# Kernel tuning notes

Hardware: AMD Instinct MI355X
Metric: run time of the kernel (lower is better)

## Reference

```python
import jax, jax.numpy as jnp
import numpy as np

N_VARS = 100_000
N_CLAUSES = 420_000
NNZ = 3 * N_CLAUSES
N_GRAPHS = 32
FM = 64
QM = 64
ROUNDS = 8
EPS = 1e-6


def _dense_init(key, din, dout):
    lim = float(np.sqrt(6.0 / (din + dout)))
    W = jax.random.uniform(key, (din, dout), jnp.float32, -lim, lim)
    return W, jnp.zeros((dout,), jnp.float32)


def setup_inputs() -> dict:
    key = jax.random.key(0)
    ks = jax.random.split(key, 16)
    # sparse literal-clause incidence: 3 literals per clause (3-SAT)
    lit_idx = jax.random.randint(ks[0], (NNZ,), 0, 2 * N_VARS)
    clause_idx = jnp.repeat(jnp.arange(N_CLAUSES), 3)
    # graph membership (batched formulas), contiguous per graph
    var_gid = jnp.sort(jax.random.randint(ks[1], (N_VARS,), 0, N_GRAPHS))
    clause_gid = jnp.sort(jax.random.randint(ks[2], (N_CLAUSES,), 0, N_GRAPHS))
    inp = {"lit_idx": lit_idx, "clause_idx": clause_idx,
           "var_gid": var_gid, "clause_gid": clause_gid}
    dims = {
        "vq": [(FM + 4, QM), (QM, QM)],                       # variables_query
        "cm": [(2 * FM, 2 * FM), (2 * FM, FM + QM)],          # clause_update
        "ug": [(4 * FM, 2 * FM), (2 * FM, 2 * FM), (2 * FM, FM)],  # update_gate
        "co": [(FM, FM), (FM, 1)],                             # clauses_mask_output
    }
    i = 3
    for name, layers in dims.items():
        for l, (din, dout) in enumerate(layers):
            W, b = _dense_init(ks[i], din, dout)
            i += 1
            inp[f"{name}_W{l}"] = W
            inp[f"{name}_b{l}"] = b
    return inp


def _mlp(x, params):
    for W, b in params[:-1]:
        x = jax.nn.relu(x @ W + b)
    W, b = params[-1]
    return x @ W + b


def _pair_norm(x, gid, n_graphs):
    # per-graph mean-subtract + RMS normalize (PairNorm, subtract_mean=True)
    cnt = jnp.maximum(
        jax.ops.segment_sum(jnp.ones((x.shape[0],), x.dtype), gid, num_segments=n_graphs), 1.0)[:, None]
    mean = jax.ops.segment_sum(x, gid, num_segments=n_graphs) / cnt
    x = x - mean[gid]
    var = jax.ops.segment_sum(jnp.mean(x * x, axis=-1, keepdims=True), gid, num_segments=n_graphs) / cnt
    return x * jax.lax.rsqrt(var[gid] + EPS)


def _forward(lit_idx, clause_idx, var_gid, clause_gid,
             vq_W0, vq_b0, vq_W1, vq_b1,
             cm_W0, cm_b0, cm_W1, cm_b1,
             ug_W0, ug_b0, ug_W1, ug_b1, ug_W2, ug_b2,
             co_W0, co_b0, co_W1, co_b1):
    vq = [(vq_W0, vq_b0), (vq_W1, vq_b1)]
    cm = [(cm_W0, cm_b0), (cm_W1, cm_b1)]
    ug = [(ug_W0, ug_b0), (ug_W1, ug_b1), (ug_W2, ug_b2)]
    co = [(co_W0, co_b0), (co_W1, co_b1)]
    V = var_gid.shape[0]
    C = clause_gid.shape[0]
    L = 2 * V  # literals

    variables = jnp.ones((V, FM), jnp.float32)
    clauses = jnp.ones((C, FM), jnp.float32)

    ones_e = jnp.ones((lit_idx.shape[0],), jnp.float32)
    lit_degree = jax.ops.segment_sum(ones_e, lit_idx, num_segments=L)[:, None]  # [2V,1]
    degree_weight = jax.lax.rsqrt(jnp.maximum(lit_degree, 1.0))
    var_degree_weight = 4.0 * jax.lax.rsqrt(jnp.maximum(lit_degree[:V] + lit_degree[V:], 1.0))

    def clause_loss(q):
        # softplus_loss_adj: exp(-(adj^T @ softplus([q; -q])))
        lits = jax.nn.softplus(jnp.concatenate([q, -q], axis=0))  # [2V, QM]
        cv = jax.ops.segment_sum(lits[lit_idx], clause_idx, num_segments=C)  # [C, QM]
        cl = jnp.exp(-cv)
        return jnp.sum(cl), cl

    def body(carry, key):
        variables, clauses = carry
        v1 = jnp.concatenate(
            [variables, jax.random.normal(key, (V, 4), jnp.float32)], axis=-1)
        query = _mlp(v1, vq)  # [V, QM]
        (_, clauses_loss), q_grad = jax.value_and_grad(clause_loss, has_aux=True)(query)
        variables_grad = q_grad * var_degree_weight

        clause_unit = jnp.concatenate([clauses, 4.0 * clauses_loss], axis=-1)  # [C, 2*FM]
        clause_data = _mlp(clause_unit, cm)  # [C, FM+QM]
        variables_loss_all = clause_data[:, :QM]
        new_clause = _pair_norm(clause_data[:, QM:], clause_gid, N_GRAPHS) * 0.25
        clauses = new_clause + 0.1 * clauses

        # adj @ variables_loss_all : scatter clause features to literals
        variables_loss = jax.ops.segment_sum(
            variables_loss_all[clause_idx], lit_idx, num_segments=L) * degree_weight  # [2V, QM]
        unit = jnp.concatenate(
            [variables_grad, variables, variables_loss[:V], variables_loss[V:]], axis=-1)
        new_variables = _pair_norm(_mlp(unit, ug), var_gid, N_GRAPHS) * 0.25
        variables = new_variables + 0.1 * variables

        logits = _mlp(clauses, co)  # [C, 1]
        variables = jax.lax.stop_gradient(variables) * 0.2 + variables * 0.8
        clauses = jax.lax.stop_gradient(clauses) * 0.2  # + clauses * 0.0
        return (variables, clauses), logits

    keys = jax.random.split(jax.random.key(42), ROUNDS + 1)
    (_, _), logits_seq = jax.lax.scan(body, (variables, clauses), keys[:ROUNDS])
    last_logits = logits_seq[-1]
    noise = jax.random.normal(keys[ROUNDS], last_logits.shape, jnp.float32)
    return jnp.squeeze(jax.nn.sigmoid(last_logits + noise), axis=-1)  # [C]


def reference(lit_idx, clause_idx, var_gid, clause_gid,
              vq_W0, vq_b0, vq_W1, vq_b1,
              cm_W0, cm_b0, cm_W1, cm_b1,
              ug_W0, ug_b0, ug_W1, ug_b1, ug_W2, ug_b2,
              co_W0, co_b0, co_W1, co_b1):
    return _forward(lit_idx, clause_idx, var_gid, clause_gid,
                    vq_W0, vq_b0, vq_W1, vq_b1,
                    cm_W0, cm_b0, cm_W1, cm_b1,
                    ug_W0, ug_b0, ug_W1, ug_b1, ug_W2, ug_b2,
                    co_W0, co_b0, co_W1, co_b1)
```

## Files before the change

### kernel.cpp

```cpp
#include <hip/hip_runtime.h>
#include <hip/hip_bf16.h>
#include <cstdint>
#include <cstddef>

constexpr int V_N = 100000;
constexpr int C_N = 420000;
constexpr int L_N = 2 * V_N;
constexpr int E_N = 3 * C_N;
constexpr int NGR = 32;
constexpr int NROUNDS = 8;
constexpr int SCAN_NB = (L_N + 255) / 256;

using bf16 = __hip_bfloat16;
typedef __attribute__((ext_vector_type(8))) short short8;
typedef __attribute__((ext_vector_type(4))) float float4v;

__device__ inline float b2f(bf16 h) { return __bfloat162float(h); }
__device__ inline bf16 f2b(float f) { return __float2bfloat16(f); }
__device__ inline float sb2f(short s) { return __uint_as_float(((uint32_t)(uint16_t)s) << 16); }
__device__ inline short f2sb(float f) { bf16 h = f2b(f); return *(short*)&h; }

template<typename T> __device__ inline float loadT(const T* p);
template<> __device__ inline float loadT<float>(const float* p) { return *p; }
template<> __device__ inline float loadT<bf16>(const bf16* p) { return b2f(*p); }

template<typename TX> __device__ inline void load8(const TX* p, float* v);
template<> __device__ inline void load8<bf16>(const bf16* p, float* v) {
  short8 s = *(const short8*)p;
#pragma unroll
  for (int e = 0; e < 8; e++) v[e] = sb2f(s[e]);
}
template<> __device__ inline void load8<float>(const float* p, float* v) {
  float4 a = *(const float4*)p;
  float4 b = *(const float4*)(p + 4);
  v[0] = a.x; v[1] = a.y; v[2] = a.z; v[3] = a.w;
  v[4] = b.x; v[5] = b.y; v[6] = b.z; v[7] = b.w;
}

__device__ inline float wload(const void* W, size_t idx, int isf32) {
  return isf32 ? ((const float*)W)[idx] : b2f(((const bf16*)W)[idx]);
}

__host__ __device__ inline void tf2x32(uint32_t k0, uint32_t k1,
                                       uint32_t x0, uint32_t x1,
                                       uint32_t* o0, uint32_t* o1) {
  uint32_t ks2 = k0 ^ k1 ^ 0x1BD11BDAu;
  x0 += k0; x1 += k1;
#define TFR(d) do { x0 += x1; x1 = (x1 << (d)) | (x1 >> (32 - (d))); x1 ^= x0; } while (0)
  TFR(13); TFR(15); TFR(26); TFR(6);
  x0 += k1;  x1 += ks2 + 1u;
  TFR(17); TFR(29); TFR(16); TFR(24);
  x0 += ks2; x1 += k0 + 2u;
  TFR(13); TFR(15); TFR(26); TFR(6);
  x0 += k0;  x1 += k1 + 3u;
  TFR(17); TFR(29); TFR(16); TFR(24);
  x0 += k1;  x1 += ks2 + 4u;
  TFR(13); TFR(15); TFR(26); TFR(6);
  x0 += ks2; x1 += k0 + 5u;
#undef TFR
  *o0 = x0; *o1 = x1;
}

__device__ inline uint32_t part_bits(uint32_t ka, uint32_t kb, uint32_t e) {
  uint32_t h1, h2;
  tf2x32(ka, kb, 0u, e, &h1, &h2);
  return h1 ^ h2;
}

__device__ inline float erfinv_f32(float x) {
  float w = -log1pf(-x * x);
  float p;
  if (w < 5.0f) {
    w -= 2.5f;
    p = 2.81022636e-08f;
    p = fmaf(p, w, 3.43273939e-07f);
    p = fmaf(p, w, -3.5233877e-06f);
    p = fmaf(p, w, -4.39150654e-06f);
    p = fmaf(p, w, 0.00021858087f);
    p = fmaf(p, w, -0.00125372503f);
    p = fmaf(p, w, -0.00417768164f);
    p = fmaf(p, w, 0.246640727f);
    p = fmaf(p, w, 1.50140941f);
  } else {
    w = sqrtf(w) - 3.0f;
    p = -0.000200214257f;
    p = fmaf(p, w, 0.000100950558f);
    p = fmaf(p, w, 0.00134934322f);
    p = fmaf(p, w, -0.00367342844f);
    p = fmaf(p, w, 0.00573950773f);
    p = fmaf(p, w, -0.0076224613f);
    p = fmaf(p, w, 0.00943887047f);
    p = fmaf(p, w, 1.00167406f);
    p = fmaf(p, w, 2.83297682f);
  }
  return p * x;
}

__device__ inline float normal_from_bits(uint32_t bits) {
  float u01 = __uint_as_float((bits >> 9) | 0x3f800000u) - 1.0f;
  const float lo = -0.99999994f;
  float u = u01 * 2.0f + lo;
  u = fmaxf(lo, u);
  return 1.41421356f * erfinv_f32(u);
}

__global__ void fill_f32(float* p, size_t n, float v) {
  size_t i = (size_t)blockIdx.x * blockDim.x + threadIdx.x;
  size_t stride = (size_t)gridDim.x * blockDim.x;
  for (; i < n; i += stride) p[i] = v;
}
__global__ void fill_u32(uint32_t* p, size_t n, uint32_t v) {
  size_t i = (size_t)blockIdx.x * blockDim.x + threadIdx.x;
  size_t stride = (size_t)gridDim.x * blockDim.x;
  for (; i < n; i += stride) p[i] = v;
}
__global__ void fill_b16(bf16* p, size_t n, float v) {
  size_t i = (size_t)blockIdx.x * blockDim.x + threadIdx.x;
  size_t stride = (size_t)gridDim.x * blockDim.x;
  bf16 b = f2b(v);
  for (; i < n; i += stride) p[i] = b;
}

__global__ void detect_dtype_kernel(const uint32_t* __restrict__ w, int* __restrict__ flag) {
  if (blockIdx.x == 0 && threadIdx.x == 0) {
    int votes = 0;
    for (int i = 0; i < 16; i++) {
      uint32_t lo = w[i] & 0xFFFFu;
      uint32_t e = (lo >> 7) & 0xFFu;
      if (e >= 0x70u && e < 0x80u) votes++;
    }
    *flag = (votes >= 12) ? 0 : 1;
  }
}

__global__ void pack_w_kernel(const void* __restrict__ W, const int* __restrict__ flagp,
                              int realK, int Kpad, int M, int Wld, int wcol0,
                              int srow0, float sscale, bf16* __restrict__ out) {
  int idx = blockIdx.x * 256 + threadIdx.x;
  if (idx >= Kpad * M) return;
  int j = idx & 7;
  int lane = (idx >> 3) & 63;
  int t = idx >> 9;
  int MT = M / 16;
  int kt = t / MT, nt = t - kt * MT;
  int k = kt * 32 + (lane >> 4) * 8 + j;
  int n = nt * 16 + (lane & 15);
  float v = 0.0f;
  if (k < realK) {
    v = wload(W, (size_t)k * Wld + wcol0 + n, *flagp);
    if (k >= srow0) v *= sscale;
  }
  out[idx] = f2b(v);
}

__global__ void count_deg_kernel(const int* __restrict__ lit, int* __restrict__ deg) {
  int e = blockIdx.x * 256 + threadIdx.x;
  if (e < E_N) atomicAdd(&deg[lit[e]], 1);
}

__global__ void hist32_kernel(const int* __restrict__ gid, int n, int* __restrict__ out) {
  __shared__ int bins[NGR];
  int t = threadIdx.x;
  if (t < NGR) bins[t] = 0;
  __syncthreads();
  int i = blockIdx.x * 256 + t;
  if (i < n) atomicAdd(&bins[gid[i]], 1);
  __syncthreads();
  if (t < NGR && bins[t] > 0) atomicAdd(&out[t], bins[t]);
}

__global__ void weights_kernel(const int* __restrict__ deg,
                               float* __restrict__ dw, float* __restrict__ vdw) {
  int l = blockIdx.x * 256 + threadIdx.x;
  if (l < L_N) dw[l] = rsqrtf(fmaxf((float)deg[l], 1.0f));
  if (l < V_N) vdw[l] = 4.0f * rsqrtf(fmaxf((float)(deg[l] + deg[l + V_N]), 1.0f));
}

__global__ void scan_partial_kernel(const int* __restrict__ deg, int* __restrict__ part) {
  __shared__ int red[256];
  int b = blockIdx.x, t = threadIdx.x;
  int i = b * 256 + t;
  red[t] = (i < L_N) ? deg[i] : 0;
  __syncthreads();
  for (int o = 128; o > 0; o >>= 1) {
    if (t < o) red[t] += red[t + o];
    __syncthreads();
  }
  if (t == 0) part[b] = red[0];
}

__global__ void scan_base_kernel(const int* __restrict__ part, int* __restrict__ base) {
  __shared__ int buf[SCAN_NB + 1];
  int t = threadIdx.x;
  for (int i = t; i < SCAN_NB; i += 256) buf[i] = part[i];
  __syncthreads();
  if (t == 0) {
    int acc = 0;
    for (int i = 0; i < SCAN_NB; i++) { int v = buf[i]; buf[i] = acc; acc += v; }
    buf[SCAN_NB] = acc;
  }
  __syncthreads();
  for (int i = t; i <= SCAN_NB; i += 256) base[i] = buf[i];
}

__global__ void scan_write_kernel(const int* __restrict__ deg, const int* __restrict__ base,
                                  int* __restrict__ offs) {
  __shared__ int s[256];
  int b = blockIdx.x, t = threadIdx.x;
  int i = b * 256 + t;
  int v = (i < L_N) ? deg[i] : 0;
  s[t] = v;
  __syncthreads();
  for (int o = 1; o < 256; o <<= 1) {
    int x = (t >= o) ? s[t - o] : 0;
    __syncthreads();
    s[t] += x;
    __syncthreads();
  }
  if (i < L_N) offs[i] = base[b] + s[t] - v;
  if (b == 0 && t == 0) offs[L_N] = base[SCAN_NB];
}

__global__ void csr_fill_kernel(const int* __restrict__ lit,
                                const int* __restrict__ offs, int* __restrict__ cursor,
                                int* __restrict__ csr) {
  int e = blockIdx.x * 256 + threadIdx.x;
  if (e < E_N) {
    int l = lit[e];
    int p = atomicAdd(&cursor[l], 1);
    csr[offs[l] + p] = e / 3;
  }
}


__global__ __launch_bounds__(256) void vq_fused_kernel(
    const bf16* __restrict__ variables,
    const bf16* __restrict__ W0p, const void* __restrict__ b0,
    const bf16* __restrict__ W1p, const void* __restrict__ b1,
    const int* __restrict__ flagp, uint32_t ka, uint32_t kb,
    bf16* __restrict__ SG, int N) {
  __shared__ bf16 hs[64][72];
  int tid = threadIdx.x;
  int wave = tid >> 6, lane = tid & 63, quad = lane >> 4, m16 = lane & 15;
  int row = blockIdx.x * 64 + wave * 16 + m16;
  int rowc = min(row, N - 1);
  int isf32 = *flagp;
  float4v acc[4];
#pragma unroll
  for (int nt = 0; nt < 4; nt++) acc[nt] = (float4v){0.f, 0.f, 0.f, 0.f};
  const short8* w0 = (const short8*)W0p;
  for (int k0 = 0; k0 < 96; k0 += 32) {
    int ks = k0 + quad * 8;
    short8 a;
    if (ks < 64) {
      a = *(const short8*)(variables + (size_t)rowc * 64 + ks);
    } else if (ks == 64) {
#pragma unroll
      for (int e = 0; e < 8; e++)
        a[e] = (e < 4)
             ? f2sb(normal_from_bits(part_bits(ka, kb, (uint32_t)(rowc * 4 + e))))
             : (short)0;
    } else {
      a = (short8){0, 0, 0, 0, 0, 0, 0, 0};
    }
#pragma unroll
    for (int nt = 0; nt < 4; nt++) {
      short8 b = w0[((k0 >> 5) * 4 + nt) * 64 + lane];
      acc[nt] = __builtin_amdgcn_mfma_f32_16x16x32_bf16(a, b, acc[nt], 0, 0, 0);
    }
  }
  int rl = wave * 16 + quad * 4;
#pragma unroll
  for (int nt = 0; nt < 4; nt++) {
    int col = nt * 16 + m16;
    float bv = wload(b0, col, isf32);
#pragma unroll
    for (int i = 0; i < 4; i++)
      hs[rl + i][col] = f2b(fmaxf(acc[nt][i] + bv, 0.0f));
  }
  __syncthreads();
  float4v acc2[4];
#pragma unroll
  for (int nt = 0; nt < 4; nt++) acc2[nt] = (float4v){0.f, 0.f, 0.f, 0.f};
  const short8* w1 = (const short8*)W1p;
  for (int k0 = 0; k0 < 64; k0 += 32) {
    short8 a = *(const short8*)&hs[wave * 16 + m16][k0 + quad * 8];
#pragma unroll
    for (int nt = 0; nt < 4; nt++) {
      short8 b = w1[((k0 >> 5) * 4 + nt) * 64 + lane];
      acc2[nt] = __builtin_amdgcn_mfma_f32_16x16x32_bf16(a, b, acc2[nt], 0, 0, 0);
    }
  }
  int rbase = blockIdx.x * 64 + wave * 16 + quad * 4;
#pragma unroll
  for (int nt = 0; nt < 4; nt++) {
    int col = nt * 16 + m16;
    float bv = wload(b1, col, isf32);
#pragma unroll
    for (int i = 0; i < 4; i++) {
      int r = rbase + i;
      if (r < N) {
        float q = acc2[nt][i] + bv;
        float sgn = 1.0f / (1.0f + expf(q));
        float sgp = 1.0f / (1.0f + expf(-q));
        SG[(size_t)r * 64 + col] = f2b(sgn);
        SG[(size_t)(r + V_N) * 64 + col] = f2b(sgp);
      }
    }
  }
}

__global__ __launch_bounds__(256) void cm_fused_kernel(
    const bf16* __restrict__ clauses, const bf16* __restrict__ clb,
    const bf16* __restrict__ W0p, const void* __restrict__ b0,
    const bf16* __restrict__ W1p, const void* __restrict__ b1,
    const int* __restrict__ flagp,
    bf16* __restrict__ Dl, bf16* __restrict__ Dn, int N) {
  __shared__ bf16 hs[64][136];
  int tid = threadIdx.x;
  int wave = tid >> 6, lane = tid & 63, quad = lane >> 4, m16 = lane & 15;
  int row = blockIdx.x * 64 + wave * 16 + m16;
  int rowc = min(row, N - 1);
  int isf32 = *flagp;
  float4v acc[8];
#pragma unroll
  for (int nt = 0; nt < 8; nt++) acc[nt] = (float4v){0.f, 0.f, 0.f, 0.f};
  const short8* w0 = (const short8*)W0p;
  for (int k0 = 0; k0 < 128; k0 += 32) {
    int ks = k0 + quad * 8;
    const bf16* src = (ks < 64) ? clauses + (size_t)rowc * 64 + ks
                                : clb + (size_t)rowc * 64 + (ks - 64);
    short8 a = *(const short8*)src;
#pragma unroll
    for (int nt = 0; nt < 8; nt++) {
      short8 b = w0[((k0 >> 5) * 8 + nt) * 64 + lane];
      acc[nt] = __builtin_amdgcn_mfma_f32_16x16x32_bf16(a, b, acc[nt], 0, 0, 0);
    }
  }
  int rl = wave * 16 + quad * 4;
#pragma unroll
  for (int nt = 0; nt < 8; nt++) {
    int col = nt * 16 + m16;
    float bv = wload(b0, col, isf32);
#pragma unroll
    for (int i = 0; i < 4; i++)
      hs[rl + i][col] = f2b(fmaxf(acc[nt][i] + bv, 0.0f));
  }
  __syncthreads();
#pragma unroll
  for (int nt = 0; nt < 8; nt++) acc[nt] = (float4v){0.f, 0.f, 0.f, 0.f};
  const short8* w1 = (const short8*)W1p;
  for (int k0 = 0; k0 < 128; k0 += 32) {
    short8 a = *(const short8*)&hs[wave * 16 + m16][k0 + quad * 8];
#pragma unroll
    for (int nt = 0; nt < 8; nt++) {
      short8 b = w1[((k0 >> 5) * 8 + nt) * 64 + lane];
      acc[nt] = __builtin_amdgcn_mfma_f32_16x16x32_bf16(a, b, acc[nt], 0, 0, 0);
    }
  }
  int rbase = blockIdx.x * 64 + wave * 16 + quad * 4;
#pragma unroll
  for (int nt = 0; nt < 8; nt++) {
    int col = nt * 16 + m16;
    float bv = wload(b1, col, isf32);
#pragma unroll
    for (int i = 0; i < 4; i++) {
      int r = rbase + i;
      if (r < N) {
        float v = acc[nt][i] + bv;
        if (col < 64) Dl[(size_t)r * 64 + col] = f2b(v);
        else          Dn[(size_t)r * 64 + (col - 64)] = f2b(v);
      }
    }
  }
}

__global__ __launch_bounds__(256) void ug_fused_kernel(
    const bf16* __restrict__ QG, const bf16* __restrict__ variables,
    const bf16* __restrict__ VLb,
    const bf16* __restrict__ W0p, const void* __restrict__ b0,
    const bf16* __restrict__ W1p, const void* __restrict__ b1,
    const bf16* __restrict__ W2p, const void* __restrict__ b2,
    const int* __restrict__ flagp, float* __restrict__ NV, int N) {
  __shared__ bf16 h1[64][136];
  __shared__ bf16 h2[64][136];
  int tid = threadIdx.x;
  int wave = tid >> 6, lane = tid & 63, quad = lane >> 4, m16 = lane & 15;
  int row = blockIdx.x * 64 + wave * 16 + m16;
  int rowc = min(row, N - 1);
  int isf32 = *flagp;
  int rl = wave * 16 + quad * 4;
  float4v acc[8];
#pragma unroll
  for (int nt = 0; nt < 8; nt++) acc[nt] = (float4v){0.f, 0.f, 0.f, 0.f};
  const short8* w0 = (const short8*)W0p;
  for (int k0 = 0; k0 < 256; k0 += 32) {
    int ks = k0 + quad * 8;
    const bf16* src;
    if (ks < 64)       src = QG + (size_t)rowc * 64 + ks;
    else if (ks < 128) src = variables + (size_t)rowc * 64 + (ks - 64);
    else               src = VLb + (size_t)rowc * 128 + (ks - 128);
    short8 a = *(const short8*)src;
#pragma unroll
    for (int nt = 0; nt < 8; nt++) {
      short8 b = w0[((k0 >> 5) * 8 + nt) * 64 + lane];
      acc[nt] = __builtin_amdgcn_mfma_f32_16x16x32_bf16(a, b, acc[nt], 0, 0, 0);
    }
  }
#pragma unroll
  for (int nt = 0; nt < 8; nt++) {
    int col = nt * 16 + m16;
    float bv = wload(b0, col, isf32);
#pragma unroll
    for (int i = 0; i < 4; i++)
      h1[rl + i][col] = f2b(fmaxf(acc[nt][i] + bv, 0.0f));
  }
  __syncthreads();
#pragma unroll
  for (int nt = 0; nt < 8; nt++) acc[nt] = (float4v){0.f, 0.f, 0.f, 0.f};
  const short8* w1 = (const short8*)W1p;
  for (int k0 = 0; k0 < 128; k0 += 32) {
    short8 a = *(const short8*)&h1[wave * 16 + m16][k0 + quad * 8];
#pragma unroll
    for (int nt = 0; nt < 8; nt++) {
      short8 b = w1[((k0 >> 5) * 8 + nt) * 64 + lane];
      acc[nt] = __builtin_amdgcn_mfma_f32_16x16x32_bf16(a, b, acc[nt], 0, 0, 0);
    }
  }
#pragma unroll
  for (int nt = 0; nt < 8; nt++) {
    int col = nt * 16 + m16;
    float bv = wload(b1, col, isf32);
#pragma unroll
    for (int i = 0; i < 4; i++)
      h2[rl + i][col] = f2b(fmaxf(acc[nt][i] + bv, 0.0f));
  }
  __syncthreads();
  float4v acc3[4];
#pragma unroll
  for (int nt = 0; nt < 4; nt++) acc3[nt] = (float4v){0.f, 0.f, 0.f, 0.f};
  const short8* w2 = (const short8*)W2p;
  for (int k0 = 0; k0 < 128; k0 += 32) {
    short8 a = *(const short8*)&h2[wave * 16 + m16][k0 + quad * 8];
#pragma unroll
    for (int nt = 0; nt < 4; nt++) {
      short8 b = w2[((k0 >> 5) * 4 + nt) * 64 + lane];
      acc3[nt] = __builtin_amdgcn_mfma_f32_16x16x32_bf16(a, b, acc3[nt], 0, 0, 0);
    }
  }
  int rbase = blockIdx.x * 64 + wave * 16 + quad * 4;
#pragma unroll
  for (int nt = 0; nt < 4; nt++) {
    int col = nt * 16 + m16;
    float bv = wload(b2, col, isf32);
#pragma unroll
    for (int i = 0; i < 4; i++) {
      int r = rbase + i;
      if (r < N) NV[(size_t)r * 64 + col] = acc3[nt][i] + bv;
    }
  }
}

__global__ void cl_kernel(const bf16* __restrict__ SG, const int* __restrict__ lit,
                          bf16* __restrict__ cl, float* __restrict__ stats) {
  if (blockIdx.x == 0) {
    for (int i = threadIdx.x; i < 4096; i += 256) stats[i] = 0.0f;
  }
  int t = blockIdx.x * 256 + threadIdx.x;
  int c = t >> 3, j = t & 7;
  if (c >= C_N) return;
  int l0 = lit[3 * c], l1 = lit[3 * c + 1], l2 = lit[3 * c + 2];
  short8 s0 = *(const short8*)&SG[(size_t)l0 * 64 + j * 8];
  short8 s1 = *(const short8*)&SG[(size_t)l1 * 64 + j * 8];
  short8 s2 = *(const short8*)&SG[(size_t)l2 * 64 + j * 8];
  short8 r;
#pragma unroll
  for (int e = 0; e < 8; e++)
    r[e] = f2sb(sb2f(s0[e]) * sb2f(s1[e]) * sb2f(s2[e]));
  *(short8*)&cl[(size_t)c * 64 + j * 8] = r;
}

__global__ void qgrad_kernel(const bf16* __restrict__ SG, const bf16* __restrict__ clb,
                             const int* __restrict__ csr, const int* __restrict__ offs,
                             const float* __restrict__ vdw, bf16* __restrict__ QG) {
  int t = blockIdx.x * 256 + threadIdx.x;
  int v = t >> 3, j = t & 7;
  if (v >= V_N) return;
  float gp[8], gn[8];
#pragma unroll
  for (int e = 0; e < 8; e++) { gp[e] = 0.0f; gn[e] = 0.0f; }
  int p0 = offs[v], p1 = offs[v + 1];
  for (int p = p0; p < p1; p++) {
    short8 x = *(const short8*)&clb[(size_t)csr[p] * 64 + j * 8];
#pragma unroll
    for (int e = 0; e < 8; e++) gp[e] += sb2f(x[e]);
  }
  p0 = offs[v + V_N]; p1 = offs[v + V_N + 1];
  for (int p = p0; p < p1; p++) {
    short8 x = *(const short8*)&clb[(size_t)csr[p] * 64 + j * 8];
#pragma unroll
    for (int e = 0; e < 8; e++) gn[e] += sb2f(x[e]);
  }
  short8 sgn = *(const short8*)&SG[(size_t)v * 64 + j * 8];
  short8 sgp = *(const short8*)&SG[(size_t)(v + V_N) * 64 + j * 8];
  float w = vdw[v];
  short8 r;
#pragma unroll
  for (int e = 0; e < 8; e++)
    r[e] = f2sb((-sb2f(sgp[e]) * gp[e] + sb2f(sgn[e]) * gn[e]) * w);
  *(short8*)&QG[(size_t)v * 64 + j * 8] = r;
}

__global__ void vlb_gather_kernel(const bf16* __restrict__ Dl, const int* __restrict__ csr,
                                  const int* __restrict__ offs, const float* __restrict__ dw,
                                  bf16* __restrict__ VLb, float* __restrict__ stats) {
  if (blockIdx.x == 0) {
    for (int i = threadIdx.x; i < 4096; i += 256) stats[i] = 0.0f;
  }
  int t = blockIdx.x * 256 + threadIdx.x;
  int l = t >> 3, j = t & 7;
  if (l >= L_N) return;
  float s[8];
#pragma unroll
  for (int e = 0; e < 8; e++) s[e] = 0.0f;
  int p0 = offs[l], p1 = offs[l + 1];
  for (int p = p0; p < p1; p++) {
    short8 x = *(const short8*)&Dl[(size_t)csr[p] * 64 + j * 8];
#pragma unroll
    for (int e = 0; e < 8; e++) s[e] += sb2f(x[e]);
  }
  float w = dw[l];
  size_t v = (l < V_N) ? (size_t)l : (size_t)(l - V_N);
  int col = (l < V_N) ? 0 : 64;
  short8 r;
#pragma unroll
  for (int e = 0; e < 8; e++) r[e] = f2sb(s[e] * w);
  *(short8*)&VLb[v * 128 + col + j * 8] = r;
}

template<typename TX>
__global__ void pn_stats_kernel(const TX* __restrict__ X,
                                const int* __restrict__ gid, int n,
                                float* __restrict__ S1, float* __restrict__ S2) {
  int wave = blockIdx.x * blockDim.y + threadIdx.y;
  int nw = gridDim.x * blockDim.y;
  int chunk = (n + nw - 1) / nw;
  int i0 = wave * chunk;
  if (i0 >= n) return;
  int i1 = min(n, i0 + chunk);
  int lane = threadIdx.x;
  int sub = lane >> 3, j = lane & 7;
  float a1[8], a2[8];
#pragma unroll
  for (int e = 0; e < 8; e++) { a1[e] = 0.0f; a2[e] = 0.0f; }
  int ifirst = i0 + sub;
  if (ifirst >= i1) return;
  int g = gid[ifirst];
  for (int i = ifirst; i < i1; i += 8) {
    int gi = gid[i];
    if (gi != g) {
#pragma unroll
      for (int e = 0; e < 8; e++) {
        atomicAdd(&S1[g * 64 + j * 8 + e], a1[e]);
        atomicAdd(&S2[g * 64 + j * 8 + e], a2[e]);
        a1[e] = 0.0f; a2[e] = 0.0f;
      }
      g = gi;
    }
    float x[8];
    load8(&X[(size_t)i * 64 + j * 8], x);
#pragma unroll
    for (int e = 0; e < 8; e++) { a1[e] += x[e]; a2[e] += x[e] * x[e]; }
  }
#pragma unroll
  for (int e = 0; e < 8; e++) {
    atomicAdd(&S1[g * 64 + j * 8 + e], a1[e]);
    atomicAdd(&S2[g * 64 + j * 8 + e], a2[e]);
  }
}

template<typename TX>
__global__ void pn_apply_kernel(const TX* __restrict__ X,
                                const int* __restrict__ gid, int n,
                                const int* __restrict__ cnt, const float* __restrict__ S1,
                                const float* __restrict__ S2, bf16* __restrict__ state,
                                float post) {
  int t = blockIdx.x * 256 + threadIdx.x;
  int i = t >> 3, j = t & 7;
  if (i >= n) return;
  int g = gid[i];
  float c = fmaxf((float)cnt[g], 1.0f);
  float m[8], tv = 0.0f;
#pragma unroll
  for (int e = 0; e < 8; e++) {
    m[e] = S1[g * 64 + j * 8 + e] / c;
    tv += S2[g * 64 + j * 8 + e] / c - m[e] * m[e];
  }
#pragma unroll
  for (int o = 1; o < 8; o <<= 1) tv += __shfl_xor(tv, o);
  float var = fmaxf(tv, 0.0f) * (1.0f / 64.0f);
  float rs = rsqrtf(var + 1e-6f);
  float x[8];
  load8(&X[(size_t)i * 64 + j * 8], x);
  short8 st = *(const short8*)&state[(size_t)i * 64 + j * 8];
  short8 r;
#pragma unroll
  for (int e = 0; e < 8; e++) {
    float xn = (x[e] - m[e]) * rs;
    r[e] = f2sb((xn * 0.25f + 0.1f * sb2f(st[e])) * post);
  }
  *(short8*)&state[(size_t)i * 64 + j * 8] = r;
}

__global__ __launch_bounds__(256) void co_final_kernel(
    const bf16* __restrict__ clauses, const bf16* __restrict__ W0p,
    const void* __restrict__ b0, const void* __restrict__ W1,
    const void* __restrict__ b1, const int* __restrict__ flagp,
    uint32_t ka, uint32_t kb, float* __restrict__ out) {
  int tid = threadIdx.x;
  int wave = tid >> 6, lane = tid & 63, quad = lane >> 4, m16 = lane & 15;
  int row = blockIdx.x * 64 + wave * 16 + m16;
  int rowc = min(row, C_N - 1);
  int isf32 = *flagp;
  float4v acc[4];
#pragma unroll
  for (int nt = 0; nt < 4; nt++) acc[nt] = (float4v){0.f, 0.f, 0.f, 0.f};
  const short8* w0 = (const short8*)W0p;
  for (int k0 = 0; k0 < 64; k0 += 32) {
    short8 a = *(const short8*)&clauses[(size_t)rowc * 64 + k0 + quad * 8];
#pragma unroll
    for (int nt = 0; nt < 4; nt++) {
      short8 b = w0[((k0 >> 5) * 4 + nt) * 64 + lane];
      acc[nt] = __builtin_amdgcn_mfma_f32_16x16x32_bf16(a, b, acc[nt], 0, 0, 0);
    }
  }
  float s[4] = {0.f, 0.f, 0.f, 0.f};
#pragma unroll
  for (int nt = 0; nt < 4; nt++) {
    int col = nt * 16 + m16;
    float bv = wload(b0, col, isf32);
    float w1v = wload(W1, col, isf32);
#pragma unroll
    for (int i = 0; i < 4; i++) s[i] += fmaxf(acc[nt][i] + bv, 0.0f) * w1v;
  }
#pragma unroll
  for (int o = 1; o < 16; o <<= 1) {
#pragma unroll
    for (int i = 0; i < 4; i++) s[i] += __shfl_xor(s[i], o);
  }
  if (m16 == 0) {
    int rbase = blockIdx.x * 64 + wave * 16 + quad * 4;
    float bb = wload(b1, 0, isf32);
#pragma unroll
    for (int i = 0; i < 4; i++) {
      int r = rbase + i;
      if (r < C_N) {
        float lg = s[i] + bb + normal_from_bits(part_bits(ka, kb, (uint32_t)r));
        out[r] = 1.0f / (1.0f + expf(-lg));
      }
    }
  }
}

extern "C" void kernel_launch(void* const* d_in, const int* in_sizes, int n_in,
                              void* d_out, int out_size, void* d_ws, size_t ws_size,
                              hipStream_t stream) {
  (void)in_sizes; (void)n_in; (void)out_size;
  const int* lit_idx    = (const int*)d_in[0];
  const int* var_gid    = (const int*)d_in[2];
  const int* clause_gid = (const int*)d_in[3];
  const void* vq_W0 = d_in[4];
  const void* vq_b0 = d_in[5];
  const void* vq_W1 = d_in[6];
  const void* vq_b1 = d_in[7];
  const void* cm_W0 = d_in[8];
  const void* cm_b0 = d_in[9];
  const void* cm_W1 = d_in[10];
  const void* cm_b1 = d_in[11];
  const void* ug_W0 = d_in[12];
  const void* ug_b0 = d_in[13];
  const void* ug_W1 = d_in[14];
  const void* ug_b1 = d_in[15];
  const void* ug_W2 = d_in[16];
  const void* ug_b2 = d_in[17];
  const void* co_W0 = d_in[18];
  const void* co_b0 = d_in[19];
  const void* co_W1 = d_in[20];
  const void* co_b1 = d_in[21];
  float* out = (float*)d_out;

  char* ws = (char*)d_ws;
  size_t off = 0;
  auto alloc = [&](size_t bytes) -> void* {
    void* p = ws + off;
    off = (off + bytes + 255) & ~(size_t)255;
    return p;
  };
  bf16* variables = (bf16*)alloc((size_t)V_N * 64 * 2);
  bf16* clauses   = (bf16*)alloc((size_t)C_N * 64 * 2);
  char* ZE        = (char*)alloc((size_t)C_N * 64 * 2);
  char* ZD        = (char*)alloc((size_t)C_N * 64 * 2);
  bf16* QG        = (bf16*)alloc((size_t)V_N * 64 * 2);
  int*  izone     = (int*)alloc((size_t)(2 * L_N + 64) * 4);
  int*  offs      = (int*)alloc((size_t)(L_N + 1) * 4);
  int*  csr       = (int*)alloc((size_t)E_N * 4);
  int*  spart     = (int*)alloc((size_t)(2 * SCAN_NB + 2) * 4);
  float* deg_f    = (float*)alloc((size_t)L_N * 4);
  float* vdw      = (float*)alloc((size_t)V_N * 4);
  float* stats    = (float*)alloc((size_t)4096 * 4);
  int*   wflag    = (int*)alloc(256);
  bf16* vq_W0p = (bf16*)alloc((size_t)96 * 64 * 2);
  bf16* vq_W1p = (bf16*)alloc((size_t)64 * 64 * 2);
  bf16* cm_W0p = (bf16*)alloc((size_t)128 * 128 * 2);
  bf16* cm_W1p = (bf16*)alloc((size_t)128 * 128 * 2);
  bf16* ug_W0p = (bf16*)alloc((size_t)256 * 128 * 2);
  bf16* ug_W1p = (bf16*)alloc((size_t)128 * 128 * 2);
  bf16* ug_W2p = (bf16*)alloc((size_t)128 * 64 * 2);
  bf16* co_W0p = (bf16*)alloc((size_t)64 * 64 * 2);
  size_t need = off;

  auto nb = [](int n, int per) { return (n + per - 1) / per; };

  if (ws_size < need) {
    fill_f32<<<nb(C_N, 256), 256, 0, stream>>>(out, (size_t)C_N, 0.5f);
    return;
  }

  bf16* clb = (bf16*)ZE;
  bf16* Dn  = (bf16*)ZE;
  bf16* VLb = (bf16*)ZE;
  bf16* SG  = (bf16*)ZD;
  bf16* Dl  = (bf16*)ZD;
  float* NV = (float*)ZD;

  int* deg_i  = izone;
  int* cursor = izone + L_N;
  int* cntv   = izone + 2 * L_N;
  int* cntc   = cntv + 32;
  int* sbase  = spart + SCAN_NB;
  float* S1 = stats;
  float* S2 = stats + 2048;

  uint32_t kw0[9], kw1[9];
  for (int i = 0; i < 9; i++) tf2x32(0u, 42u, 0u, (uint32_t)i, &kw0[i], &kw1[i]);

  dim3 wb(64, 4);
  const int BIG = 1 << 30;

  detect_dtype_kernel<<<1, 64, 0, stream>>>((const uint32_t*)vq_W0, wflag);
  fill_u32<<<nb(2 * L_N + 64, 256), 256, 0, stream>>>((uint32_t*)izone, (size_t)(2 * L_N + 64), 0u);
  count_deg_kernel<<<nb(E_N, 256), 256, 0, stream>>>(lit_idx, deg_i);
  hist32_kernel<<<nb(V_N, 256), 256, 0, stream>>>(var_gid, V_N, cntv);
  hist32_kernel<<<nb(C_N, 256), 256, 0, stream>>>(clause_gid, C_N, cntc);
  weights_kernel<<<nb(L_N, 256), 256, 0, stream>>>(deg_i, deg_f, vdw);
  scan_partial_kernel<<<SCAN_NB, 256, 0, stream>>>(deg_i, spart);
  scan_base_kernel<<<1, 256, 0, stream>>>(spart, sbase);
  scan_write_kernel<<<SCAN_NB, 256, 0, stream>>>(deg_i, sbase, offs);
  csr_fill_kernel<<<nb(E_N, 256), 256, 0, stream>>>(lit_idx, offs, cursor, csr);
  fill_b16<<<2048, 256, 0, stream>>>(variables, (size_t)V_N * 64, 1.0f);
  fill_b16<<<2048, 256, 0, stream>>>(clauses, (size_t)C_N * 64, 1.0f);
  pack_w_kernel<<<nb(96 * 64, 256), 256, 0, stream>>>(vq_W0, wflag, 68, 96, 64, 64, 0, BIG, 1.f, vq_W0p);
  pack_w_kernel<<<nb(64 * 64, 256), 256, 0, stream>>>(vq_W1, wflag, 64, 64, 64, 64, 0, BIG, 1.f, vq_W1p);
  pack_w_kernel<<<nb(128 * 128, 256), 256, 0, stream>>>(cm_W0, wflag, 128, 128, 128, 128, 0, 64, 4.f, cm_W0p);
  pack_w_kernel<<<nb(128 * 128, 256), 256, 0, stream>>>(cm_W1, wflag, 128, 128, 128, 128, 0, BIG, 1.f, cm_W1p);
  pack_w_kernel<<<nb(256 * 128, 256), 256, 0, stream>>>(ug_W0, wflag, 256, 256, 128, 128, 0, BIG, 1.f, ug_W0p);
  pack_w_kernel<<<nb(128 * 128, 256), 256, 0, stream>>>(ug_W1, wflag, 128, 128, 128, 128, 0, BIG, 1.f, ug_W1p);
  pack_w_kernel<<<nb(128 * 64, 256), 256, 0, stream>>>(ug_W2, wflag, 128, 128, 64, 64, 0, BIG, 1.f, ug_W2p);
  pack_w_kernel<<<nb(64 * 64, 256), 256, 0, stream>>>(co_W0, wflag, 64, 64, 64, 64, 0, BIG, 1.f, co_W0p);

  for (int r = 0; r < NROUNDS; r++) {
    vq_fused_kernel<<<nb(V_N, 64), 256, 0, stream>>>(
        variables, vq_W0p, vq_b0, vq_W1p, vq_b1, wflag, kw0[r], kw1[r], SG, V_N);
    cl_kernel<<<nb(C_N * 8, 256), 256, 0, stream>>>(SG, lit_idx, clb, stats);
    qgrad_kernel<<<nb(V_N * 8, 256), 256, 0, stream>>>(SG, clb, csr, offs, vdw, QG);
    cm_fused_kernel<<<nb(C_N, 64), 256, 0, stream>>>(
        clauses, clb, cm_W0p, cm_b0, cm_W1p, cm_b1, wflag, Dl, Dn, C_N);
    pn_stats_kernel<bf16><<<128, wb, 0, stream>>>(Dn, clause_gid, C_N, S1, S2);
    pn_apply_kernel<bf16><<<nb(C_N * 8, 256), 256, 0, stream>>>(
        Dn, clause_gid, C_N, cntc, S1, S2, clauses, (r == NROUNDS - 1) ? 1.0f : 0.2f);
    vlb_gather_kernel<<<nb(L_N * 8, 256), 256, 0, stream>>>(Dl, csr, offs, deg_f, VLb, stats);
    ug_fused_kernel<<<nb(V_N, 64), 256, 0, stream>>>(
        QG, variables, VLb, ug_W0p, ug_b0, ug_W1p, ug_b1, ug_W2p, ug_b2,
        wflag, NV, V_N);
    pn_stats_kernel<float><<<128, wb, 0, stream>>>(NV, var_gid, V_N, S1, S2);
    pn_apply_kernel<float><<<nb(V_N * 8, 256), 256, 0, stream>>>(
        NV, var_gid, V_N, cntv, S1, S2, variables, 1.0f);
  }
  co_final_kernel<<<nb(C_N, 64), 256, 0, stream>>>(
      clauses, co_W0p, co_b0, co_W1, co_b1, wflag, kw0[8], kw1[8], out);
}
```

Measured before the change: 4.023 ms.

## Merge independent pair-norm stats/apply passes into combined multi-role kernel launches

Independent kernels are merged by partitioning the grid by block index. The vlb gather shares a launch with the clause pair-norm stats, and the clause pair-norm apply shares a launch with the variable stats. This takes out two launches per round and lets independent work run concurrently. To make that possible, SG/VLb move to a new dedicated buffer and the stats are split into separate clause and variable regions, so buffers that were previously aliased no longer collide. The cost is extra memory and heterogeneous blocks within one launch.

Result: no change. 3.969 ms (-1.3%).

```diff
diff --git a/kernel.cpp b/kernel.cpp
--- a/kernel.cpp
+++ b/kernel.cpp
@@ -301,10 +301,8 @@
       int r = rbase + i;
       if (r < N) {
         float q = acc2[nt][i] + bv;
-        float sgn = 1.0f / (1.0f + expf(q));
-        float sgp = 1.0f / (1.0f + expf(-q));
-        SG[(size_t)r * 64 + col] = f2b(sgn);
-        SG[(size_t)(r + V_N) * 64 + col] = f2b(sgp);
+        SG[(size_t)r * 64 + col] = f2b(1.0f / (1.0f + expf(q)));
+        SG[(size_t)(r + V_N) * 64 + col] = f2b(1.0f / (1.0f + expf(-q)));
       }
     }
   }
@@ -461,12 +459,12 @@
   }
 }
 
-__global__ void cl_kernel(const bf16* __restrict__ SG, const int* __restrict__ lit,
-                          bf16* __restrict__ cl, float* __restrict__ stats) {
-  if (blockIdx.x == 0) {
-    for (int i = threadIdx.x; i < 4096; i += 256) stats[i] = 0.0f;
-  }
-  int t = blockIdx.x * 256 + threadIdx.x;
+__device__ inline void cl_body(int bidx, const bf16* SG, const int* lit,
+                               bf16* cl, float* statsC) {
+  if (bidx == 0) {
+    for (int i = threadIdx.x; i < 4096; i += 256) statsC[i] = 0.0f;
+  }
+  int t = bidx * 256 + threadIdx.x;
   int c = t >> 3, j = t & 7;
   if (c >= C_N) return;
   int l0 = lit[3 * c], l1 = lit[3 * c + 1], l2 = lit[3 * c + 2];
@@ -480,6 +478,11 @@
   *(short8*)&cl[(size_t)c * 64 + j * 8] = r;
 }
 
+__global__ void cl_kernel(const bf16* __restrict__ SG, const int* __restrict__ lit,
+                          bf16* __restrict__ cl, float* __restrict__ statsC) {
+  cl_body(blockIdx.x, SG, lit, cl, statsC);
+}
+
 __global__ void qgrad_kernel(const bf16* __restrict__ SG, const bf16* __restrict__ clb,
                              const int* __restrict__ csr, const int* __restrict__ offs,
                              const float* __restrict__ vdw, bf16* __restrict__ QG) {
@@ -511,13 +514,13 @@
   *(short8*)&QG[(size_t)v * 64 + j * 8] = r;
 }
 
-__global__ void vlb_gather_kernel(const bf16* __restrict__ Dl, const int* __restrict__ csr,
-                                  const int* __restrict__ offs, const float* __restrict__ dw,
-                                  bf16* __restrict__ VLb, float* __restrict__ stats) {
-  if (blockIdx.x == 0) {
-    for (int i = threadIdx.x; i < 4096; i += 256) stats[i] = 0.0f;
-  }
-  int t = blockIdx.x * 256 + threadIdx.x;
+__device__ inline void vlb_body(int bidx, const bf16* Dl, const int* csr,
+                                const int* offs, const float* dw,
+                                bf16* VLb, float* statsV) {
+  if (bidx == 0) {
+    for (int i = threadIdx.x; i < 4096; i += 256) statsV[i] = 0.0f;
+  }
+  int t = bidx * 256 + threadIdx.x;
   int l = t >> 3, j = t & 7;
   if (l >= L_N) return;
   float s[8];
@@ -539,16 +542,13 @@
 }
 
 template<typename TX>
-__global__ void pn_stats_kernel(const TX* __restrict__ X,
-                                const int* __restrict__ gid, int n,
-                                float* __restrict__ S1, float* __restrict__ S2) {
-  int wave = blockIdx.x * blockDim.y + threadIdx.y;
-  int nw = gridDim.x * blockDim.y;
+__device__ inline void pn_stats_body(const TX* X, const int* gid, int n,
+                                     float* S1, float* S2, int wave, int nw) {
   int chunk = (n + nw - 1) / nw;
   int i0 = wave * chunk;
   if (i0 >= n) return;
   int i1 = min(n, i0 + chunk);
-  int lane = threadIdx.x;
+  int lane = threadIdx.x & 63;
   int sub = lane >> 3, j = lane & 7;
   float a1[8], a2[8];
 #pragma unroll
@@ -580,12 +580,10 @@
 }
 
 template<typename TX>
-__global__ void pn_apply_kernel(const TX* __restrict__ X,
-                                const int* __restrict__ gid, int n,
-                                const int* __restrict__ cnt, const float* __restrict__ S1,
-                                const float* __restrict__ S2, bf16* __restrict__ state,
-                                float post) {
-  int t = blockIdx.x * 256 + threadIdx.x;
+__device__ inline void pn_apply_body(int bidx, const TX* X, const int* gid, int n,
+                                     const int* cnt, const float* S1, const float* S2,
+                                     bf16* state, float post) {
+  int t = bidx * 256 + threadIdx.x;
   int i = t >> 3, j = t & 7;
   if (i >= n) return;
   int g = gid[i];
@@ -610,6 +608,43 @@
     r[e] = f2sb((xn * 0.25f + 0.1f * sb2f(st[e])) * post);
   }
   *(short8*)&state[(size_t)i * 64 + j * 8] = r;
+}
+
+__global__ void vlb_statsc_kernel(const bf16* __restrict__ Dl, const int* __restrict__ csr,
+                                  const int* __restrict__ offs, const float* __restrict__ dw,
+                                  bf16* __restrict__ VLb, float* __restrict__ statsV,
+                                  const bf16* __restrict__ Dn, const int* __restrict__ cgid,
+                                  float* __restrict__ S1c, float* __restrict__ S2c,
+                                  int VLBB) {
+  if (blockIdx.x < VLBB) {
+    vlb_body(blockIdx.x, Dl, csr, offs, dw, VLb, statsV);
+  } else {
+    int sb = blockIdx.x - VLBB;
+    int wave = sb * 4 + (threadIdx.x >> 6);
+    pn_stats_body<bf16>(Dn, cgid, C_N, S1c, S2c, wave, 512);
+  }
+}
+
+__global__ void applyc_statsv_kernel(const bf16* __restrict__ Dn, const int* __restrict__ cgid,
+                                     const int* __restrict__ cntc, const float* __restrict__ S1c,
+                                     const float* __restrict__ S2c, bf16* __restrict__ clauses,
+                                     float post,
+                                     const float* __restrict__ NV, const int* __restrict__ vgid,
+                                     float* __restrict__ S1v, float* __restrict__ S2v,
+                                     int AB) {
+  if (blockIdx.x < AB) {
+    pn_apply_body<bf16>(blockIdx.x, Dn, cgid, C_N, cntc, S1c, S2c, clauses, post);
+  } else {
+    int sb = blockIdx.x - AB;
+    int wave = sb * 4 + (threadIdx.x >> 6);
+    pn_stats_body<float>(NV, vgid, V_N, S1v, S2v, wave, 512);
+  }
+}
+
+__global__ void pn_apply_v_kernel(const float* __restrict__ NV, const int* __restrict__ vgid,
+                                  const int* __restrict__ cntv, const float* __restrict__ S1v,
+                                  const float* __restrict__ S2v, bf16* __restrict__ variables) {
+  pn_apply_body<float>(blockIdx.x, NV, vgid, V_N, cntv, S1v, S2v, variables, 1.0f);
 }
 
 __global__ __launch_bounds__(256) void co_final_kernel(
@@ -700,6 +735,7 @@
   bf16* clauses   = (bf16*)alloc((size_t)C_N * 64 * 2);
   char* ZE        = (char*)alloc((size_t)C_N * 64 * 2);
   char* ZD        = (char*)alloc((size_t)C_N * 64 * 2);
+  char* ZS        = (char*)alloc((size_t)L_N * 64 * 2);
   bf16* QG        = (bf16*)alloc((size_t)V_N * 64 * 2);
   int*  izone     = (int*)alloc((size_t)(2 * L_N + 64) * 4);
   int*  offs      = (int*)alloc((size_t)(L_N + 1) * 4);
@@ -707,7 +743,7 @@
   int*  spart     = (int*)alloc((size_t)(2 * SCAN_NB + 2) * 4);
   float* deg_f    = (float*)alloc((size_t)L_N * 4);
   float* vdw      = (float*)alloc((size_t)V_N * 4);
-  float* stats    = (float*)alloc((size_t)4096 * 4);
+  float* stats    = (float*)alloc((size_t)8192 * 4);
   int*   wflag    = (int*)alloc(256);
   bf16* vq_W0p = (bf16*)alloc((size_t)96 * 64 * 2);
   bf16* vq_W1p = (bf16*)alloc((size_t)64 * 64 * 2);
@@ -728,24 +764,30 @@
 
   bf16* clb = (bf16*)ZE;
   bf16* Dn  = (bf16*)ZE;
-  bf16* VLb = (bf16*)ZE;
-  bf16* SG  = (bf16*)ZD;
   bf16* Dl  = (bf16*)ZD;
   float* NV = (float*)ZD;
+  bf16* SG  = (bf16*)ZS;
+  bf16* VLb = (bf16*)ZS;
 
   int* deg_i  = izone;
   int* cursor = izone + L_N;
   int* cntv   = izone + 2 * L_N;
   int* cntc   = cntv + 32;
   int* sbase  = spart + SCAN_NB;
-  float* S1 = stats;
-  float* S2 = stats + 2048;
+  float* S1c = stats;
+  float* S2c = stats + 2048;
+  float* S1v = stats + 4096;
+  float* S2v = stats + 6144;
+  float* statsC = S1c;
+  float* statsV = S1v;
 
   uint32_t kw0[9], kw1[9];
   for (int i = 0; i < 9; i++) tf2x32(0u, 42u, 0u, (uint32_t)i, &kw0[i], &kw1[i]);
 
-  dim3 wb(64, 4);
   const int BIG = 1 << 30;
+  const int VLBB = nb(L_N * 8, 256);
+  const int AB   = nb(C_N * 8, 256);
+  const int SB   = 128;
 
   detect_dtype_kernel<<<1, 64, 0, stream>>>((const uint32_t*)vq_W0, wflag);
   fill_u32<<<nb(2 * L_N + 64, 256), 256, 0, stream>>>((uint32_t*)izone, (size_t)(2 * L_N + 64), 0u);
@@ -771,20 +813,20 @@
   for (int r = 0; r < NROUNDS; r++) {
     vq_fused_kernel<<<nb(V_N, 64), 256, 0, stream>>>(
         variables, vq_W0p, vq_b0, vq_W1p, vq_b1, wflag, kw0[r], kw1[r], SG, V_N);
-    cl_kernel<<<nb(C_N * 8, 256), 256, 0, stream>>>(SG, lit_idx, clb, stats);
+    cl_kernel<<<nb(C_N * 8, 256), 256, 0, stream>>>(SG, lit_idx, clb, statsC);
     qgrad_kernel<<<nb(V_N * 8, 256), 256, 0, stream>>>(SG, clb, csr, offs, vdw, QG);
     cm_fused_kernel<<<nb(C_N, 64), 256, 0, stream>>>(
         clauses, clb, cm_W0p, cm_b0, cm_W1p, cm_b1, wflag, Dl, Dn, C_N);
-    pn_stats_kernel<bf16><<<128, wb, 0, stream>>>(Dn, clause_gid, C_N, S1, S2);
-    pn_apply_kernel<bf16><<<nb(C_N * 8, 256), 256, 0, stream>>>(
-        Dn, clause_gid, C_N, cntc, S1, S2, clauses, (r == NROUNDS - 1) ? 1.0f : 0.2f);
-    vlb_gather_kernel<<<nb(L_N * 8, 256), 256, 0, stream>>>(Dl, csr, offs, deg_f, VLb, stats);
+    vlb_statsc_kernel<<<VLBB + SB, 256, 0, stream>>>(
+        Dl, csr, offs, deg_f, VLb, statsV, Dn, clause_gid, S1c, S2c, VLBB);
     ug_fused_kernel<<<nb(V_N, 64), 256, 0, stream>>>(
         QG, variables, VLb, ug_W0p, ug_b0, ug_W1p, ug_b1, ug_W2p, ug_b2,
         wflag, NV, V_N);
-    pn_stats_kernel<float><<<128, wb, 0, stream>>>(NV, var_gid, V_N, S1, S2);
-    pn_apply_kernel<float><<<nb(V_N * 8, 256), 256, 0, stream>>>(
-        NV, var_gid, V_N, cntv, S1, S2, variables, 1.0f);
+    applyc_statsv_kernel<<<AB + SB, 256, 0, stream>>>(
+        Dn, clause_gid, cntc, S1c, S2c, clauses, (r == NROUNDS - 1) ? 1.0f : 0.2f,
+        NV, var_gid, S1v, S2v, AB);
+    pn_apply_v_kernel<<<nb(V_N * 8, 256), 256, 0, stream>>>(
+        NV, var_gid, cntv, S1v, S2v, variables);
   }
   co_final_kernel<<<nb(C_N, 64), 256, 0, stream>>>(
       clauses, co_W0p, co_b0, co_W1, co_b1, wflag, kw0[8], kw1[8], out);
```
